# Kernel tuning notes

Measured on AMD Instinct MI355X. Metric: run time of the kernel, lower is better.

## Reference

```python
import jax, jax.numpy as jnp
import numpy as np

N_NODES = 100000
N_EDGES = 1000000
N_BATCH = 64
D = 64            # node/edge/global feature dim
IN_DIM = 3 * D    # node + agg_received_edges + global
LATENT = 32
OUT_DIM = 64


def setup_inputs() -> dict:
    key = jax.random.key(0)
    ks = jax.random.split(key, 9)
    return {
        "node_attr": jax.random.normal(ks[0], (N_NODES, D), dtype=jnp.float32),
        "edge_attr": jax.random.normal(ks[1], (N_EDGES, D), dtype=jnp.float32),
        "global_attr": jax.random.normal(ks[2], (N_BATCH, D), dtype=jnp.float32),
        "W1": jax.random.normal(ks[3], (IN_DIM, LATENT), dtype=jnp.float32) * (1.0 / np.sqrt(IN_DIM)),
        "b1": jnp.zeros((LATENT,), dtype=jnp.float32),
        "W2": jax.random.normal(ks[4], (LATENT, OUT_DIM), dtype=jnp.float32) * (1.0 / np.sqrt(LATENT)),
        "b2": jnp.zeros((OUT_DIM,), dtype=jnp.float32),
        "receivers_idx": jax.random.randint(ks[5], (N_EDGES,), 0, N_NODES, dtype=jnp.int32),
        "ng_index": jax.random.randint(ks[6], (N_NODES,), 0, N_BATCH, dtype=jnp.int32),
    }


def scatter_mean(src, index, num_segments):
    # segment-sum then divide by count (count clamped to 1 where empty -> mean=0)
    sums = jax.ops.segment_sum(src, index, num_segments=num_segments)
    cnt = jax.ops.segment_sum(jnp.ones((src.shape[0],), src.dtype), index,
                              num_segments=num_segments)
    return sums / jnp.maximum(cnt, 1.0)[:, None]


def reference(node_attr, edge_attr, global_attr, W1, b1, W2, b2,
              receivers_idx, ng_index):
    num_nodes = node_attr.shape[0]
    # aggregated received-edge features per node  [N, D]
    agg_received = scatter_mean(edge_attr, receivers_idx, num_nodes)
    # gather per-node global attrs               [N, D]
    expanded_global = global_attr[ng_index]
    # concat -> small MLP                        [N, 3D] -> [N, out_dim]
    collected = jnp.concatenate([node_attr, agg_received, expanded_global], axis=-1)
    h = jax.nn.relu(collected @ W1 + b1)
    return h @ W2 + b2
```

## Files before the change

kernel.cpp:

```cpp
#include <hip/hip_runtime.h>

#define DD 64
#define LATENT 32
#define OUTD 64
#define CAP 64

typedef float vfloat4 __attribute__((ext_vector_type(4)));

__global__ __launch_bounds__(256) void bin_kernel(
    const int* __restrict__ recv, int* __restrict__ counts,
    int* __restrict__ slots, int nEdges)
{
    int t = blockIdx.x * 256 + threadIdx.x;
    int e0 = t * 4;
    if (e0 + 3 < nEdges) {
        int4 r4 = *(const int4*)(recv + e0);
        int rank;
        rank = atomicAdd(&counts[r4.x], 1); if (rank < CAP) slots[((size_t)r4.x << 6) + rank] = e0;
        rank = atomicAdd(&counts[r4.y], 1); if (rank < CAP) slots[((size_t)r4.y << 6) + rank] = e0 + 1;
        rank = atomicAdd(&counts[r4.z], 1); if (rank < CAP) slots[((size_t)r4.z << 6) + rank] = e0 + 2;
        rank = atomicAdd(&counts[r4.w], 1); if (rank < CAP) slots[((size_t)r4.w << 6) + rank] = e0 + 3;
    } else {
        for (int e = e0; e < nEdges; ++e) {
            int r = recv[e];
            int rank = atomicAdd(&counts[r], 1);
            if (rank < CAP) slots[((size_t)r << 6) + rank] = e;
        }
    }
}

__global__ __launch_bounds__(256) void g1_kernel(
    const float* __restrict__ global_attr,
    const float* __restrict__ W1,
    const float* __restrict__ b1,
    float*       __restrict__ g1,
    int nBatch)
{
    int t = blockIdx.x * 256 + threadIdx.x;
    int b = t >> 5;
    int j = t & 31;
    if (b >= nBatch) return;
    float acc = b1[j];
    const float* g = global_attr + (size_t)b * DD;
    const float* w = W1 + 128 * LATENT + j;
    for (int k = 0; k < DD; ++k)
        acc = fmaf(g[k], w[k * LATENT], acc);
    g1[b * LATENT + j] = acc;
}

__global__ __launch_bounds__(128) void fused_kernel(
    const float* __restrict__ edge_attr,
    const int*   __restrict__ slots,
    const int*   __restrict__ counts,
    const float* __restrict__ node_attr,
    const int*   __restrict__ ng_index,
    const float* __restrict__ W1,
    const float* __restrict__ W2,
    const float* __restrict__ b2,
    const float* __restrict__ g1,
    float*       __restrict__ out,
    int nNodes)
{
    __shared__ float slab[2][64 * 65];

    const int wave = threadIdx.x >> 6;
    const int lane = threadIdx.x & 63;
    const int base = blockIdx.x * 128 + wave * 64;
    if (base >= nNodes) return;
    const int nv = min(64, nNodes - base);
    float* S = slab[wave];
    const int g = lane >> 4;
    const int s = lane & 15;

    float h[LATENT];
    {
        const int n = base + (lane < nv ? lane : 0);
        const int gb = ng_index[n];
        const vfloat4* gp = (const vfloat4*)(g1 + gb * LATENT);
#pragma unroll
        for (int q = 0; q < 8; ++q) {
            vfloat4 gv = gp[q];
            h[4*q+0] = gv.x; h[4*q+1] = gv.y;
            h[4*q+2] = gv.z; h[4*q+3] = gv.w;
        }
    }

    int cnt_n  = counts[base];
    int myid_n = slots[((size_t)base << 6) + lane];
    for (int r = 0; r < nv; ++r) {
        const int cnt  = cnt_n;
        const int myid = myid_n;
        if (r + 1 < nv) {
            cnt_n  = counts[base + r + 1];
            myid_n = slots[((size_t)(base + r + 1) << 6) + lane];
        }
        const int lim = min(cnt, CAP);

        vfloat4 acc = {0.f, 0.f, 0.f, 0.f};
        for (int i = 0; i < lim; i += 16) {
            int ia  = min(i + g,      lim - 1);
            int ib  = min(i + 4 + g,  lim - 1);
            int ic  = min(i + 8 + g,  lim - 1);
            int id_ = min(i + 12 + g, lim - 1);
            int eA = __shfl(myid, ia, 64);
            int eB = __shfl(myid, ib, 64);
            int eC = __shfl(myid, ic, 64);
            int eD = __shfl(myid, id_, 64);
            vfloat4 a = {0.f,0.f,0.f,0.f}, b = a, c = a, d = a;
            if (i + g < lim)
                a = __builtin_nontemporal_load(((const vfloat4*)(edge_attr + (size_t)eA * DD)) + s);
            if (i + 4 + g < lim)
                b = __builtin_nontemporal_load(((const vfloat4*)(edge_attr + (size_t)eB * DD)) + s);
            if (i + 8 + g < lim)
                c = __builtin_nontemporal_load(((const vfloat4*)(edge_attr + (size_t)eC * DD)) + s);
            if (i + 12 + g < lim)
                d = __builtin_nontemporal_load(((const vfloat4*)(edge_attr + (size_t)eD * DD)) + s);
            acc += a; acc += b; acc += c; acc += d;
        }
        acc.x += __shfl_xor(acc.x, 16, 64);
        acc.y += __shfl_xor(acc.y, 16, 64);
        acc.z += __shfl_xor(acc.z, 16, 64);
        acc.w += __shfl_xor(acc.w, 16, 64);
        acc.x += __shfl_xor(acc.x, 32, 64);
        acc.y += __shfl_xor(acc.y, 32, 64);
        acc.z += __shfl_xor(acc.z, 32, 64);
        acc.w += __shfl_xor(acc.w, 32, 64);

        if (g == 0) {
            float inv = 1.0f / (float)max(cnt, 1);
            S[r * 65 + 4*s + 0] = acc.x * inv;
            S[r * 65 + 4*s + 1] = acc.y * inv;
            S[r * 65 + 4*s + 2] = acc.z * inv;
            S[r * 65 + 4*s + 3] = acc.w * inv;
        }
    }

    {
        const float* w = W1 + DD * LATENT;
#pragma unroll 8
        for (int k = 0; k < DD; ++k) {
            float x = S[lane * 65 + k];
            const float* wr = w + k * LATENT;
#pragma unroll
            for (int j = 0; j < LATENT; ++j)
                h[j] = fmaf(x, wr[j], h[j]);
        }
    }

#pragma unroll 8
    for (int r = 0; r < nv; ++r)
        S[r * 65 + lane] = node_attr[(size_t)(base + r) * DD + lane];
    {
        const float* w = W1;
#pragma unroll 8
        for (int k = 0; k < DD; ++k) {
            float x = S[lane * 65 + k];
            const float* wr = w + k * LATENT;
#pragma unroll
            for (int j = 0; j < LATENT; ++j)
                h[j] = fmaf(x, wr[j], h[j]);
        }
    }

#pragma unroll
    for (int j = 0; j < LATENT; ++j) h[j] = fmaxf(h[j], 0.0f);

#pragma unroll
    for (int c = 0; c < 2; ++c) {
        float o[32];
#pragma unroll
        for (int t = 0; t < 32; ++t) o[t] = b2[c * 32 + t];
        for (int j = 0; j < LATENT; ++j) {
            const float hj = h[j];
            const float* wr = W2 + j * OUTD + c * 32;
#pragma unroll
            for (int t = 0; t < 32; ++t) o[t] = fmaf(hj, wr[t], o[t]);
        }
#pragma unroll
        for (int t = 0; t < 32; ++t) S[lane * 65 + c * 32 + t] = o[t];
    }

#pragma unroll 8
    for (int r = 0; r < nv; ++r)
        out[(size_t)(base + r) * DD + lane] = S[r * 65 + lane];
}

extern "C" void kernel_launch(void* const* d_in, const int* in_sizes, int n_in,
                              void* d_out, int out_size, void* d_ws, size_t ws_size,
                              hipStream_t stream)
{
    const float* node_attr   = (const float*)d_in[0];
    const float* edge_attr   = (const float*)d_in[1];
    const float* global_attr = (const float*)d_in[2];
    const float* W1          = (const float*)d_in[3];
    const float* b1          = (const float*)d_in[4];
    const float* W2          = (const float*)d_in[5];
    const float* b2          = (const float*)d_in[6];
    const int*   recv        = (const int*)d_in[7];
    const int*   ng_index    = (const int*)d_in[8];
    float*       out         = (float*)d_out;

    const int nNodes = in_sizes[0] / DD;
    const int nEdges = in_sizes[1] / DD;
    const int nBatch = in_sizes[2] / DD;

    int*   counts = (int*)d_ws;
    int*   slots  = counts + nNodes;
    float* g1     = (float*)(slots + (size_t)nNodes * CAP);

    hipMemsetAsync(counts, 0, (size_t)nNodes * sizeof(int), stream);

    bin_kernel<<<(nEdges + 1023) / 1024, 256, 0, stream>>>(recv, counts, slots, nEdges);

    g1_kernel<<<(nBatch * LATENT + 255) / 256, 256, 0, stream>>>(
        global_attr, W1, b1, g1, nBatch);

    fused_kernel<<<(nNodes + 127) / 128, 128, 0, stream>>>(
        edge_attr, slots, counts, node_attr, ng_index, W1, W2, b2, g1, out, nNodes);
}
```

Before: 485.0 us.

## Merge bin and g1 launches, load slot ids lazily, prefetch node rows

Folds the global-projection kernel into the binning kernel as extra blocks, which removes one launch. In the fused kernel, each node's slot-id row is now read 16 entries at a time and only as far as the node's count, instead of all 64 lanes eagerly. That cuts slot traffic since nodes average about 10 edges. Node-attribute rows are preloaded into 64 registers with nontemporal loads before the first matmul, and outputs use nontemporal stores. The 64-element register array may raise register pressure and lower occupancy.

```diff
diff --git a/kernel.cpp b/kernel.cpp
--- a/kernel.cpp
+++ b/kernel.cpp
@@ -7,11 +7,30 @@
 
 typedef float vfloat4 __attribute__((ext_vector_type(4)));
 
-__global__ __launch_bounds__(256) void bin_kernel(
-    const int* __restrict__ recv, int* __restrict__ counts,
-    int* __restrict__ slots, int nEdges)
+__global__ __launch_bounds__(256) void bin_g1_kernel(
+    const int*   __restrict__ recv, int* __restrict__ counts,
+    int*         __restrict__ slots, int nEdges, int edgeBlocks,
+    const float* __restrict__ global_attr,
+    const float* __restrict__ W1,
+    const float* __restrict__ b1,
+    float*       __restrict__ g1,
+    int nBatch)
 {
-    int t = blockIdx.x * 256 + threadIdx.x;
+    const int bid = blockIdx.x;
+    if (bid >= edgeBlocks) {
+        int t = (bid - edgeBlocks) * 256 + threadIdx.x;
+        int b = t >> 5;
+        int j = t & 31;
+        if (b >= nBatch) return;
+        float acc = b1[j];
+        const float* g = global_attr + (size_t)b * DD;
+        const float* w = W1 + 128 * LATENT + j;
+        for (int k = 0; k < DD; ++k)
+            acc = fmaf(g[k], w[k * LATENT], acc);
+        g1[b * LATENT + j] = acc;
+        return;
+    }
+    int t = bid * 256 + threadIdx.x;
     int e0 = t * 4;
     if (e0 + 3 < nEdges) {
         int4 r4 = *(const int4*)(recv + e0);
@@ -27,25 +46,6 @@
             if (rank < CAP) slots[((size_t)r << 6) + rank] = e;
         }
     }
-}
-
-__global__ __launch_bounds__(256) void g1_kernel(
-    const float* __restrict__ global_attr,
-    const float* __restrict__ W1,
-    const float* __restrict__ b1,
-    float*       __restrict__ g1,
-    int nBatch)
-{
-    int t = blockIdx.x * 256 + threadIdx.x;
-    int b = t >> 5;
-    int j = t & 31;
-    if (b >= nBatch) return;
-    float acc = b1[j];
-    const float* g = global_attr + (size_t)b * DD;
-    const float* w = W1 + 128 * LATENT + j;
-    for (int k = 0; k < DD; ++k)
-        acc = fmaf(g[k], w[k * LATENT], acc);
-    g1[b * LATENT + j] = acc;
 }
 
 __global__ __launch_bounds__(128) void fused_kernel(
@@ -69,8 +69,9 @@
     if (base >= nNodes) return;
     const int nv = min(64, nNodes - base);
     float* S = slab[wave];
-    const int g = lane >> 4;
-    const int s = lane & 15;
+    const int g  = lane >> 4;
+    const int s  = lane & 15;
+    const int l16 = lane & 15;
 
     float h[LATENT];
     {
@@ -86,22 +87,24 @@
     }
 
     int cnt_n  = counts[base];
-    int myid_n = slots[((size_t)base << 6) + lane];
+    int myid_n = slots[((size_t)base << 6) + l16];
     for (int r = 0; r < nv; ++r) {
-        const int cnt  = cnt_n;
-        const int myid = myid_n;
+        const int cnt = cnt_n;
+        int myid = myid_n;
         if (r + 1 < nv) {
             cnt_n  = counts[base + r + 1];
-            myid_n = slots[((size_t)(base + r + 1) << 6) + lane];
+            myid_n = slots[((size_t)(base + r + 1) << 6) + l16];
         }
         const int lim = min(cnt, CAP);
 
         vfloat4 acc = {0.f, 0.f, 0.f, 0.f};
         for (int i = 0; i < lim; i += 16) {
-            int ia  = min(i + g,      lim - 1);
-            int ib  = min(i + 4 + g,  lim - 1);
-            int ic  = min(i + 8 + g,  lim - 1);
-            int id_ = min(i + 12 + g, lim - 1);
+            if (i > 0)
+                myid = slots[((size_t)(base + r) << 6) + i + l16];
+            int ia  = min(i + g,      lim - 1) - i;
+            int ib  = min(i + 4 + g,  lim - 1) - i;
+            int ic  = min(i + 8 + g,  lim - 1) - i;
+            int id_ = min(i + 12 + g, lim - 1) - i;
             int eA = __shfl(myid, ia, 64);
             int eB = __shfl(myid, ib, 64);
             int eC = __shfl(myid, ic, 64);
@@ -135,6 +138,12 @@
         }
     }
 
+    float na[64];
+#pragma unroll
+    for (int r = 0; r < 64; ++r)
+        if (r < nv)
+            na[r] = __builtin_nontemporal_load(node_attr + (size_t)(base + r) * DD + lane);
+
     {
         const float* w = W1 + DD * LATENT;
 #pragma unroll 8
@@ -147,9 +156,10 @@
         }
     }
 
-#pragma unroll 8
-    for (int r = 0; r < nv; ++r)
-        S[r * 65 + lane] = node_attr[(size_t)(base + r) * DD + lane];
+#pragma unroll
+    for (int r = 0; r < 64; ++r)
+        if (r < nv)
+            S[r * 65 + lane] = na[r];
     {
         const float* w = W1;
 #pragma unroll 8
@@ -182,7 +192,8 @@
 
 #pragma unroll 8
     for (int r = 0; r < nv; ++r)
-        out[(size_t)(base + r) * DD + lane] = S[r * 65 + lane];
+        __builtin_nontemporal_store(S[r * 65 + lane],
+                                    out + (size_t)(base + r) * DD + lane);
 }
 
 extern "C" void kernel_launch(void* const* d_in, const int* in_sizes, int n_in,
@@ -210,9 +221,10 @@
 
     hipMemsetAsync(counts, 0, (size_t)nNodes * sizeof(int), stream);
 
-    bin_kernel<<<(nEdges + 1023) / 1024, 256, 0, stream>>>(recv, counts, slots, nEdges);
-
-    g1_kernel<<<(nBatch * LATENT + 255) / 256, 256, 0, stream>>>(
+    const int edgeBlocks = (nEdges + 1023) / 1024;
+    const int g1Blocks   = (nBatch * LATENT + 255) / 256;
+    bin_g1_kernel<<<edgeBlocks + g1Blocks, 256, 0, stream>>>(
+        recv, counts, slots, nEdges, edgeBlocks,
         global_attr, W1, b1, g1, nBatch);
 
     fused_kernel<<<(nNodes + 127) / 128, 128, 0, stream>>>(
```

After: 508.3 us. 4.8% more time.
